# Kernel optimization log

Hardware: AMD Instinct MI355X
Metric: run time of the kernel (lower is better)

Reference implementation:

```python
import jax, jax.numpy as jnp
import numpy as np

B, N = 8, 32
V, W_DIM, H_DIM, EMBED, NSTATE = 10000, 512, 512, 256, 30


def _lstm_dir(seq, Wih, Whh, bih, bhh):
    # seq: [M, T, w] -> [M, T, h]; PyTorch gate order i, f, g, o
    M = seq.shape[0]
    H = Whh.shape[1]
    bias = bih + bhh

    def step(carry, x_t):
        h, c = carry
        gates = x_t @ Wih.T + h @ Whh.T + bias
        i, f, g, o = jnp.split(gates, 4, axis=-1)
        c = jax.nn.sigmoid(f) * c + jax.nn.sigmoid(i) * jnp.tanh(g)
        h = jax.nn.sigmoid(o) * jnp.tanh(c)
        return (h, c), h

    init = (jnp.zeros((M, H), seq.dtype), jnp.zeros((M, H), seq.dtype))
    _, hs = jax.lax.scan(step, init, jnp.swapaxes(seq, 0, 1))
    return jnp.swapaxes(hs, 0, 1)


def setup_inputs() -> dict:
    key = jax.random.key(0)
    ks = jax.random.split(key, 8)
    sc = 1.0 / np.sqrt(H_DIM)
    nrm = lambda k, shape, s: jax.random.normal(k, shape, dtype=jnp.float32) * s
    return {
        "x": jax.random.randint(ks[0], (B, N), 0, V, dtype=jnp.int32),
        "lengths": jnp.full((B,), N, dtype=jnp.int32),
        "emb": nrm(ks[1], (V, W_DIM), 0.02),
        "Wih_f": nrm(ks[2], (4 * H_DIM, W_DIM), sc),
        "Whh_f": nrm(ks[3], (4 * H_DIM, H_DIM), sc),
        "bih_f": jnp.zeros((4 * H_DIM,), jnp.float32),
        "bhh_f": jnp.zeros((4 * H_DIM,), jnp.float32),
        "Wih_b": nrm(ks[4], (4 * H_DIM, W_DIM), sc),
        "Whh_b": nrm(ks[5], (4 * H_DIM, H_DIM), sc),
        "bih_b": jnp.zeros((4 * H_DIM,), jnp.float32),
        "bhh_b": jnp.zeros((4 * H_DIM,), jnp.float32),
        "Wout": nrm(ks[6], (NSTATE * EMBED, 2 * H_DIM), 1.0 / np.sqrt(2 * H_DIM)),
        "bout": jnp.zeros((NSTATE * EMBED,), jnp.float32),
    }


def reference(x, lengths, emb, Wih_f, Whh_f, bih_f, bhh_f,
              Wih_b, Whh_b, bih_b, bhh_b, Wout, bout):
    word_emb = emb[x]  # [B, N, w]
    chunks = []
    for k in range(1, N):  # loop over span lengths, as in the original
        # windows of length k+1 starting at each position: [N-k, k+1]
        idx = jnp.arange(k + 1)[None, :] + jnp.arange(N - k)[:, None]
        span = word_emb[:, idx].reshape(B * (N - k), k + 1, W_DIM)
        fwd = _lstm_dir(span, Wih_f, Whh_f, bih_f, bhh_f)
        bwd = _lstm_dir(span[:, ::-1], Wih_b, Whh_b, bih_b, bhh_b)[:, ::-1]
        h = jnp.concatenate([fwd, bwd], axis=-1)  # [M, k+1, 2h]
        out = h @ Wout.T + bout                   # [M, k+1, NSTATE*EMBED]
        out = out.reshape(B, N - k, k + 1, NSTATE, EMBED).mean(axis=2)
        chunks.append(out)
    # spans laid out by increasing length: [B, N(N-1)/2, NSTATE, EMBED]
    return jnp.concatenate(chunks, axis=1)
```

## Files before the change

### kernel.cpp

```cpp
#include <hip/hip_runtime.h>
#include <hip/hip_bf16.h>


#define BT __hip_bfloat16

typedef short bf16x8 __attribute__((ext_vector_type(8)));
typedef float f32x4 __attribute__((ext_vector_type(4)));

__device__ __forceinline__ bf16x8 ld_frag(const BT* p) {
    return *reinterpret_cast<const bf16x8*>(p);
}
__device__ __forceinline__ f32x4 mfma16(bf16x8 a, bf16x8 b, f32x4 c) {
    return __builtin_amdgcn_mfma_f32_16x16x32_bf16(a, b, c, 0, 0, 0);
}
__device__ __forceinline__ float sigm(float x) { return 1.0f / (1.0f + __expf(-x)); }
__device__ __forceinline__ float tanhfast(float x) {
    float e = __expf(-2.0f * fabsf(x));
    float r = (1.0f - e) / (1.0f + e);
    return copysignf(r, x);
}

__device__ __forceinline__ bf16x8 ld_sys16(const BT* p) {
    bf16x8 r;
    asm volatile("global_load_dwordx4 %0, %1, off sc0 sc1"
                 : "=v"(r) : "v"(p) : "memory");
    return r;
}
__device__ __forceinline__ void st_sys_short(BT* p, BT v) {
    union { BT b; unsigned short u; } t; t.b = v;
    unsigned int d = t.u;
    asm volatile("global_store_short %0, %1, off sc0 sc1"
                 :: "v"(p), "v"(d) : "memory");
}
__device__ __forceinline__ void st_sys_u32(unsigned int* p, unsigned int v) {
    asm volatile("global_store_dword %0, %1, off sc0 sc1"
                 :: "v"(p), "v"(v) : "memory");
}
__device__ __forceinline__ unsigned int ld_sys_u32(const unsigned int* p) {
    unsigned int r;
    asm volatile("global_load_dword %0, %1, off sc0 sc1\n\t"
                 "s_waitcnt vmcnt(0)"
                 : "=v"(r) : "v"(p) : "memory");
    return r;
}

__device__ __forceinline__ void async16(const BT* g, BT* l) {
    __builtin_amdgcn_global_load_lds(
        (const __attribute__((address_space(1))) unsigned int*)g,
        (__attribute__((address_space(3))) unsigned int*)l,
        16, 0, 0);
}

union B4 { BT b[4]; unsigned long long u; };

__global__ __launch_bounds__(256) void conv_kernel(
    const float* __restrict__ s0, const float* __restrict__ s1,
    const float* __restrict__ s2, const float* __restrict__ s3,
    const float* __restrict__ s4, BT* __restrict__ dbase)
{
    const int z = blockIdx.z;
    const float* src = (z == 0) ? s0 : (z == 1) ? s1 : (z == 2) ? s2 : (z == 3) ? s3 : s4;
    const int nel = (z == 4) ? 7864320 : 1048576;
    BT* dst = dbase + (long)z * 1048576;
    const int n4 = nel >> 2;
    for (int i = blockIdx.x * 256 + threadIdx.x; i < n4; i += gridDim.x * 256) {
        float4 v = reinterpret_cast<const float4*>(src)[i];
        B4 t;
        t.b[0] = __float2bfloat16(v.x); t.b[1] = __float2bfloat16(v.y);
        t.b[2] = __float2bfloat16(v.z); t.b[3] = __float2bfloat16(v.w);
        reinterpret_cast<unsigned long long*>(dst)[i] = t.u;
    }
}

__global__ __launch_bounds__(256) void gather_kernel(
    const int* __restrict__ x, const float* __restrict__ emb, BT* __restrict__ Xemb)
{
    const int i = blockIdx.x * 256 + threadIdx.x;
    const int r = i >> 7;
    const int cq = i & 127;
    const long row = x[r];
    float4 v = reinterpret_cast<const float4*>(emb + row * 512)[cq];
    B4 t;
    t.b[0] = __float2bfloat16(v.x); t.b[1] = __float2bfloat16(v.y);
    t.b[2] = __float2bfloat16(v.z); t.b[3] = __float2bfloat16(v.w);
    reinterpret_cast<unsigned long long*>(Xemb + (long)r * 512)[cq] = t.u;
}

__global__ __launch_bounds__(256) void gx_kernel(
    const BT* __restrict__ Xemb,
    const BT* __restrict__ WihF, const BT* __restrict__ WihB,
    const float* __restrict__ bih_f, const float* __restrict__ bhh_f,
    const float* __restrict__ bih_b, const float* __restrict__ bhh_b,
    float* __restrict__ Gx, unsigned int* __restrict__ flags)
{
    const int dir = blockIdx.z;
    const BT* Wih = dir ? WihB : WihF;
    const float* bih = dir ? bih_b : bih_f;
    const float* bhh = dir ? bhh_b : bhh_f;
    float* G = Gx + (long)dir * 256 * 2048;

    const int tid = threadIdx.x;
    const int w = tid >> 6, lane = tid & 63;
    const int m = lane & 15, q = lane >> 4;
    const int r0 = blockIdx.x * 32;
    const int c0 = blockIdx.y * 128 + w * 32;

    if (tid == 0)
        st_sys_u32(&flags[(blockIdx.z * 8 + blockIdx.x) * 16 + blockIdx.y], 0u);

    const BT* a0p = Xemb + (long)(r0 + m) * 512 + q * 8;
    const BT* a1p = Xemb + (long)(r0 + 16 + m) * 512 + q * 8;
    const BT* b0p = Wih + (long)(c0 + m) * 512 + q * 8;
    const BT* b1p = Wih + (long)(c0 + 16 + m) * 512 + q * 8;

    f32x4 acc[2][2] = {};
    for (int k0 = 0; k0 < 512; k0 += 32) {
        bf16x8 a0 = ld_frag(a0p + k0);
        bf16x8 a1 = ld_frag(a1p + k0);
        bf16x8 b0 = ld_frag(b0p + k0);
        bf16x8 b1 = ld_frag(b1p + k0);
        acc[0][0] = mfma16(a0, b0, acc[0][0]);
        acc[0][1] = mfma16(a0, b1, acc[0][1]);
        acc[1][0] = mfma16(a1, b0, acc[1][0]);
        acc[1][1] = mfma16(a1, b1, acc[1][1]);
    }
    #pragma unroll
    for (int rt = 0; rt < 2; ++rt)
        #pragma unroll
        for (int ct = 0; ct < 2; ++ct)
            #pragma unroll
            for (int reg = 0; reg < 4; ++reg) {
                int r = r0 + rt * 16 + q * 4 + reg;
                int c = c0 + ct * 16 + m;
                G[(long)r * 2048 + c] = acc[rt][ct][reg] + bih[c] + bhh[c];
            }
}

__global__ __launch_bounds__(256, 1) void rec_kernel(
    const BT* __restrict__ WhhF, const BT* __restrict__ WhhB,
    const float* __restrict__ Gx,
    BT* __restrict__ H0, BT* __restrict__ H1,
    float* __restrict__ C, float* __restrict__ S,
    BT* __restrict__ Apack, unsigned int* __restrict__ flags)
{
    const int dir = blockIdx.z;
    const int tid = threadIdx.x;
    const int w = tid >> 6, lane = tid & 63;
    const int m = lane & 15, q = lane >> 4;

    const BT* W = dir ? WhhB : WhhF;
    const float* G = Gx + (long)dir * 256 * 2048;
    BT* Ha = H0 + (long)dir * 256 * 512;
    BT* Hb = H1 + (long)dir * 256 * 512;
    float* Cd = C + (long)dir * 256 * 512;
    float* Sd = S + (long)dir * 256 * 512;

    const int r0 = blockIdx.x * 32;
    const int u0 = blockIdx.y * 32;
    unsigned int* flg = flags + (dir * 8 + blockIdx.x) * 16;
    const int myy = blockIdx.y;

    const BT* b0p = W + (long)(w * 512 + u0 + m) * 512 + q * 8;
    const BT* b1p = W + (long)(w * 512 + u0 + 16 + m) * 512 + q * 8;
    bf16x8 wb0[16], wb1[16];
    #pragma unroll
    for (int kk = 0; kk < 16; ++kk) {
        wb0[kk] = ld_frag(b0p + kk * 32);
        wb1[kk] = ld_frag(b1p + kk * 32);
    }

    __shared__ float gbuf[4][32][33];
    __shared__ BT hbuf[32 * 512];

    const int srow = tid >> 3;
    const int sch0 = tid & 7;
    const int xr = m & 7;

    for (int s = 0; s < 32; ++s) {
        const BT* Hi = (s & 1) ? Hb : Ha;
        BT* Ho = (s & 1) ? Ha : Hb;
        if (r0 < 8 * (s + 1)) {
            const BT* hsrc = Hi + (long)(r0 + srow) * 512;
            bf16x8 hv[8];
            #pragma unroll
            for (int rr = 0; rr < 8; ++rr)
                hv[rr] = ld_sys16(hsrc + (sch0 + rr * 8) * 8);
            asm volatile("s_waitcnt vmcnt(0)" ::: "memory");
            __builtin_amdgcn_sched_barrier(0);
            #pragma unroll
            for (int rr = 0; rr < 8; ++rr) {
                const int ch = sch0 + rr * 8;
                *reinterpret_cast<bf16x8*>(
                    hbuf + srow * 512 + (ch ^ (srow & 7)) * 8) = hv[rr];
            }
            __syncthreads();

            f32x4 acc[2][2] = {};
            #pragma unroll
            for (int kk = 0; kk < 16; ++kk) {
                const int sl = (((kk << 2) | q) ^ xr) * 8;
                bf16x8 a0 = *reinterpret_cast<const bf16x8*>(hbuf + m * 512 + sl);
                bf16x8 a1 = *reinterpret_cast<const bf16x8*>(hbuf + (16 + m) * 512 + sl);
                acc[0][0] = mfma16(a0, wb0[kk], acc[0][0]);
                acc[0][1] = mfma16(a0, wb1[kk], acc[0][1]);
                acc[1][0] = mfma16(a1, wb0[kk], acc[1][0]);
                acc[1][1] = mfma16(a1, wb1[kk], acc[1][1]);
            }
            #pragma unroll
            for (int rt = 0; rt < 2; ++rt)
                #pragma unroll
                for (int ct = 0; ct < 2; ++ct)
                    #pragma unroll
                    for (int reg = 0; reg < 4; ++reg)
                        gbuf[w][rt * 16 + q * 4 + reg][ct * 16 + m] = acc[rt][ct][reg];
            __syncthreads();

            const int pos = dir ? (31 - s) : s;
            for (int idx = tid; idx < 1024; idx += 256) {
                const int r = idx >> 5, ul = idx & 31;
                const int chain = r0 + r;
                const int d = chain >> 3;
                const int b = chain & 7;
                if (d > s) continue;
                const int u = u0 + ul;
                const float* gx = G + (long)(b * 32 + pos) * 2048 + u;
                const float gi = gbuf[0][r][ul] + gx[0];
                const float gf = gbuf[1][r][ul] + gx[512];
                const float gg = gbuf[2][r][ul] + gx[1024];
                const float go = gbuf[3][r][ul] + gx[1536];
                const long o = (long)chain * 512 + u;
                const float c_new = sigm(gf) * Cd[o] + sigm(gi) * tanhfast(gg);
                const float h = sigm(go) * tanhfast(c_new);
                Cd[o] = c_new;
                st_sys_short(Ho + o, __float2bfloat16(h));
                const float s_new = Sd[o] + h;
                Sd[o] = s_new;
                const int k = s - d;
                if (k >= 1) {
                    const int p_span = dir ? pos : d;
                    const int off = (k - 1) * 32 - ((k - 1) * k) / 2;
                    Apack[(long)(b * 496 + off + p_span) * 1024 + dir * 512 + u] =
                        __float2bfloat16(s_new * __builtin_amdgcn_rcpf((float)(k + 1)));
                }
            }
        }
        if (s == 31) break;

        asm volatile("s_waitcnt vmcnt(0)" ::: "memory");
        __syncthreads();
        if (tid == 0)
            st_sys_u32(&flg[myy], (unsigned)(s + 1));
        if (tid < 16) {
            const unsigned int tgt = (unsigned)(s + 1);
            while (ld_sys_u32(&flg[tid]) < tgt)
                __builtin_amdgcn_s_sleep(1);
        }
        __syncthreads();
        asm volatile("" ::: "memory");
    }
}

__global__ __launch_bounds__(256) void proj_kernel(
    const BT* __restrict__ Apack, const BT* __restrict__ Woutbf,
    const float* __restrict__ bout, float* __restrict__ out)
{
    __shared__ BT As[128 * 64];
    __shared__ BT Bs[128 * 64];

    const int tid = threadIdx.x;
    const int lane = tid & 63;
    const int wu = __builtin_amdgcn_readfirstlane(tid >> 6);
    const int m = lane & 15, q = lane >> 4;
    const int wr = wu >> 1, wc = wu & 1;
    const int r0 = blockIdx.x * 128;
    const int c0 = blockIdx.y * 128;

    const int srow = lane >> 3;
    const int schunk = (lane & 7) ^ srow;

    f32x4 acc[4][4] = {};

    for (int kc = 0; kc < 16; ++kc) {
        const int k0 = kc * 64;
        #pragma unroll
        for (int j = 0; j < 4; ++j) {
            const int L = wu * 4 + j;
            const int row = L * 8 + srow;
            async16(Apack + (long)(r0 + row) * 1024 + k0 + schunk * 8,
                    As + L * 512);
            async16(Woutbf + (long)(c0 + row) * 1024 + k0 + schunk * 8,
                    Bs + L * 512);
        }
        __syncthreads();
        #pragma unroll
        for (int ks = 0; ks < 2; ++ks) {
            const int slot = ((ks << 2) | q) ^ (m & 7);
            bf16x8 af[4], bf[4];
            #pragma unroll
            for (int t = 0; t < 4; ++t) {
                af[t] = ld_frag(As + (wr * 64 + t * 16 + m) * 64 + slot * 8);
                bf[t] = ld_frag(Bs + (wc * 64 + t * 16 + m) * 64 + slot * 8);
            }
            #pragma unroll
            for (int mt = 0; mt < 4; ++mt)
                #pragma unroll
                for (int nt = 0; nt < 4; ++nt)
                    acc[mt][nt] = mfma16(af[mt], bf[nt], acc[mt][nt]);
        }
        __syncthreads();
    }

    #pragma unroll
    for (int mt = 0; mt < 4; ++mt)
        #pragma unroll
        for (int nt = 0; nt < 4; ++nt)
            #pragma unroll
            for (int reg = 0; reg < 4; ++reg) {
                const int r = r0 + wr * 64 + mt * 16 + q * 4 + reg;
                const int c = c0 + wc * 64 + nt * 16 + m;
                out[(long)r * 7680 + c] = acc[mt][nt][reg] + bout[c];
            }
}

extern "C" void kernel_launch(void* const* d_in, const int* in_sizes, int n_in,
                              void* d_out, int out_size, void* d_ws, size_t ws_size,
                              hipStream_t stream) {
    const int*   x     = (const int*)d_in[0];
    const float* emb   = (const float*)d_in[2];
    const float* Wih_f = (const float*)d_in[3];
    const float* Whh_f = (const float*)d_in[4];
    const float* bih_f = (const float*)d_in[5];
    const float* bhh_f = (const float*)d_in[6];
    const float* Wih_b = (const float*)d_in[7];
    const float* Whh_b = (const float*)d_in[8];
    const float* bih_b = (const float*)d_in[9];
    const float* bhh_b = (const float*)d_in[10];
    const float* Wout  = (const float*)d_in[11];
    const float* bout  = (const float*)d_in[12];
    float* out = (float*)d_out;

    char* ws = (char*)d_ws;
    const long MB = 1 << 20;
    float* Gx    = (float*)(ws + 0);
    BT*    H0    = (BT*)(ws + 4 * MB);
    BT*    H1    = (BT*)(ws + 4 * MB + 512 * 1024);
    float* C     = (float*)(ws + 5 * MB);
    float* S     = (float*)(ws + 6 * MB);
    BT*    Apack = (BT*)(ws + 7 * MB);
    BT*    Xemb  = (BT*)(ws + 7 * MB + 7936 * 1024);
    BT*    Wbf   = (BT*)(ws + 15 * MB);
    BT*    WihF  = Wbf;
    BT*    WihB  = Wbf + 1048576;
    BT*    WhhF  = Wbf + 2 * 1048576;
    BT*    WhhB  = Wbf + 3 * 1048576;
    BT*    Woutb = Wbf + 4 * 1048576;
    unsigned int* flags = (unsigned int*)(ws + 38 * MB);

    hipMemsetAsync(ws + 4 * MB, 0, 3 * MB, stream);

    conv_kernel<<<dim3(512, 1, 5), 256, 0, stream>>>(
        Wih_f, Wih_b, Whh_f, Whh_b, Wout, Wbf);
    gather_kernel<<<128, 256, 0, stream>>>(x, emb, Xemb);

    gx_kernel<<<dim3(8, 16, 2), 256, 0, stream>>>(
        Xemb, WihF, WihB, bih_f, bhh_f, bih_b, bhh_b, Gx, flags);

    {
        void* args[] = {
            (void*)&WhhF, (void*)&WhhB, (void*)&Gx,
            (void*)&H0, (void*)&H1, (void*)&C, (void*)&S,
            (void*)&Apack, (void*)&flags
        };
        hipLaunchCooperativeKernel((const void*)rec_kernel, dim3(8, 16, 2),
                                   dim3(256, 1, 1), args, 0, stream);
    }

    proj_kernel<<<dim3(31, 60), 256, 0, stream>>>(Apack, Woutb, bout, out);
}
```

Measured before the change: 496.4 us.

## Signal step flag before running-sum and Apack stores in recurrent kernel

Splits the recurrent LSTM step so the new hidden state is written and the completion flag is published before the running-sum update and the Apack span-mean stores. This overlaps that non-critical global write traffic with other blocks' barrier wait instead of keeping it on the critical path. It also replaces the cooperative launch with a plain launch to avoid cooperative-launch overhead. The risk is that the grid-wide spin barrier now depends on all 256 blocks being co-resident without a guarantee from the runtime.

```diff
diff --git a/kernel.cpp b/kernel.cpp
--- a/kernel.cpp
+++ b/kernel.cpp
@@ -179,7 +179,11 @@
     for (int s = 0; s < 32; ++s) {
         const BT* Hi = (s & 1) ? Hb : Ha;
         BT* Ho = (s & 1) ? Ha : Hb;
-        if (r0 < 8 * (s + 1)) {
+        const bool active = (r0 < 8 * (s + 1));
+        const int pos = dir ? (31 - s) : s;
+        float hreg[4];
+
+        if (active) {
             const BT* hsrc = Hi + (long)(r0 + srow) * 512;
             bf16x8 hv[8];
             #pragma unroll
@@ -215,8 +219,9 @@
                         gbuf[w][rt * 16 + q * 4 + reg][ct * 16 + m] = acc[rt][ct][reg];
             __syncthreads();
 
-            const int pos = dir ? (31 - s) : s;
-            for (int idx = tid; idx < 1024; idx += 256) {
+            #pragma unroll
+            for (int j = 0; j < 4; ++j) {
+                const int idx = tid + j * 256;
                 const int r = idx >> 5, ul = idx & 31;
                 const int chain = r0 + r;
                 const int d = chain >> 3;
@@ -233,7 +238,29 @@
                 const float h = sigm(go) * tanhfast(c_new);
                 Cd[o] = c_new;
                 st_sys_short(Ho + o, __float2bfloat16(h));
-                const float s_new = Sd[o] + h;
+                hreg[j] = h;
+            }
+        }
+
+        if (s < 31) {
+            asm volatile("s_waitcnt vmcnt(0)" ::: "memory");
+            __syncthreads();
+            if (tid == 0)
+                st_sys_u32(&flg[myy], (unsigned)(s + 1));
+        }
+
+        if (active) {
+            #pragma unroll
+            for (int j = 0; j < 4; ++j) {
+                const int idx = tid + j * 256;
+                const int r = idx >> 5, ul = idx & 31;
+                const int chain = r0 + r;
+                const int d = chain >> 3;
+                const int b = chain & 7;
+                if (d > s) continue;
+                const int u = u0 + ul;
+                const long o = (long)chain * 512 + u;
+                const float s_new = Sd[o] + hreg[j];
                 Sd[o] = s_new;
                 const int k = s - d;
                 if (k >= 1) {
@@ -244,19 +271,16 @@
                 }
             }
         }
-        if (s == 31) break;
-
-        asm volatile("s_waitcnt vmcnt(0)" ::: "memory");
-        __syncthreads();
-        if (tid == 0)
-            st_sys_u32(&flg[myy], (unsigned)(s + 1));
-        if (tid < 16) {
-            const unsigned int tgt = (unsigned)(s + 1);
-            while (ld_sys_u32(&flg[tid]) < tgt)
-                __builtin_amdgcn_s_sleep(1);
-        }
-        __syncthreads();
-        asm volatile("" ::: "memory");
+
+        if (s < 31) {
+            if (tid < 16) {
+                const unsigned int tgt = (unsigned)(s + 1);
+                while (ld_sys_u32(&flg[tid]) < tgt)
+                    __builtin_amdgcn_s_sleep(1);
+            }
+            __syncthreads();
+            asm volatile("" ::: "memory");
+        }
     }
 }
 
@@ -365,15 +389,8 @@
     gx_kernel<<<dim3(8, 16, 2), 256, 0, stream>>>(
         Xemb, WihF, WihB, bih_f, bhh_f, bih_b, bhh_b, Gx, flags);
 
-    {
-        void* args[] = {
-            (void*)&WhhF, (void*)&WhhB, (void*)&Gx,
-            (void*)&H0, (void*)&H1, (void*)&C, (void*)&S,
-            (void*)&Apack, (void*)&flags
-        };
-        hipLaunchCooperativeKernel((const void*)rec_kernel, dim3(8, 16, 2),
-                                   dim3(256, 1, 1), args, 0, stream);
-    }
+    rec_kernel<<<dim3(8, 16, 2), 256, 0, stream>>>(
+        WhhF, WhhB, Gx, H0, H1, C, S, Apack, flags);
 
     proj_kernel<<<dim3(31, 60), 256, 0, stream>>>(Apack, Woutb, bout, out);
 }
```

Measured after the change: 456.1 us. -8.1%, faster.
